# Kernel optimization log

Measured on AMD Instinct MI355X. Metric: run time of the kernel, lower is better.

## Reference

```python
import jax, jax.numpy as jnp
import numpy as np

C = 96        # d_model
DI = 192      # d_inner = 2*C
N = 16        # d_state
R = 6         # dt_rank = ceil(C/16)
K = 4         # scan directions
B_, H_, W_ = 2, 48, 48


def setup_inputs():
    key = jax.random.key(0)
    ks = jax.random.split(key, 12)
    def rn(k, shape, s=0.02):
        return jax.random.normal(k, shape, jnp.float32) * s
    # S4D-real A init and realistic dt bias (inverse softplus of dt in [1e-3, 1e-1])
    A = jnp.tile(jnp.arange(1, N + 1, dtype=jnp.float32), (K, DI, 1))
    dt = jax.random.uniform(ks[0], (K, DI), jnp.float32, 1e-3, 1e-1)
    inv_softplus_dt = dt + jnp.log(-jnp.expm1(-dt))
    return {
        "x": jax.random.normal(ks[1], (B_, C, H_, W_), jnp.float32),
        "ln1_w": jnp.ones((C,), jnp.float32), "ln1_b": jnp.zeros((C,), jnp.float32),
        "in_proj_w": rn(ks[2], (2 * DI, C)),
        "conv_w": rn(ks[3], (DI, 1, 3, 3), 0.1), "conv_b": jnp.zeros((DI,), jnp.float32),
        "x_proj_w": rn(ks[4], (K, R + 2 * N, DI)),
        "dt_proj_w": rn(ks[5], (K, DI, R), 0.1), "dt_proj_b": inv_softplus_dt,
        "A_log": jnp.log(A), "Ds": jnp.ones((K, DI), jnp.float32),
        "out_norm_w": jnp.ones((DI,), jnp.float32), "out_norm_b": jnp.zeros((DI,), jnp.float32),
        "out_proj_w": rn(ks[6], (C, DI)),
        "ln2_w": jnp.ones((C,), jnp.float32), "ln2_b": jnp.zeros((C,), jnp.float32),
        "fc1_w": rn(ks[7], (C, C)), "fc1_b": jnp.zeros((C,), jnp.float32),
        "fc2_w": rn(ks[8], (C, C)), "fc2_b": jnp.zeros((C,), jnp.float32),
        "proj_w": rn(ks[9], (1, C)), "proj_b": jnp.zeros((1,), jnp.float32),
    }


def _layernorm(x, w, b, eps=1e-5):
    mu = x.mean(-1, keepdims=True)
    var = x.var(-1, keepdims=True)
    return (x - mu) * jax.lax.rsqrt(var + eps) * w + b


def _selective_scan(u, delta, A, Bm, Cm, D):
    # u, delta: (B,K,D,L); A: (K,D,N); Bm, Cm: (B,K,N,L); D: (K,D)
    dA = jnp.exp(jnp.einsum('bkdl,kdn->lbkdn', delta, A))
    dBu = jnp.einsum('bkdl,bknl->lbkdn', delta * u, Bm)
    Ct = jnp.moveaxis(Cm, -1, 0)  # (L,B,K,N)
    h0 = jnp.zeros(dA.shape[1:], u.dtype)
    def step(h, inp):
        dA_t, dBu_t, C_t = inp
        h = dA_t * h + dBu_t
        y = jnp.einsum('bkdn,bkn->bkd', h, C_t)
        return h, y
    _, ys = jax.lax.scan(step, h0, (dA, dBu, Ct))
    y = jnp.moveaxis(ys, 0, -1)  # (B,K,D,L)
    return y + u * D[None, :, :, None]


def _ss2d(x, in_proj_w, conv_w, conv_b, x_proj_w, dt_proj_w, dt_proj_b,
          A_log, Ds, out_norm_w, out_norm_b, out_proj_w):
    Bsz, H, W, _ = x.shape
    L = H * W
    xz = x @ in_proj_w.T                      # (B,H,W,2*DI)
    xh, z = jnp.split(xz, 2, axis=-1)
    xc = xh.transpose(0, 3, 1, 2)             # (B,DI,H,W)
    xc = jax.lax.conv_general_dilated(
        xc, conv_w, (1, 1), ((1, 1), (1, 1)),
        feature_group_count=DI,
        dimension_numbers=('NCHW', 'OIHW', 'NCHW')) + conv_b[None, :, None, None]
    xc = jax.nn.silu(xc)
    # cross-scan: 4 directions (row-major, col-major, and their reverses)
    xf = xc.reshape(Bsz, DI, L)
    xt = xc.transpose(0, 1, 3, 2).reshape(Bsz, DI, L)
    xs2 = jnp.stack([xf, xt], axis=1)
    xs = jnp.concatenate([xs2, jnp.flip(xs2, axis=-1)], axis=1)   # (B,4,DI,L)
    x_dbl = jnp.einsum('bkdl,kcd->bkcl', xs, x_proj_w)
    dts, Bm, Cm = jnp.split(x_dbl, [R, R + N], axis=2)
    delta = jnp.einsum('bkrl,kdr->bkdl', dts, dt_proj_w) + dt_proj_b[None, :, :, None]
    delta = jax.nn.softplus(delta)
    A = -jnp.exp(A_log)
    out_y = _selective_scan(xs, delta, A, Bm, Cm, Ds)             # (B,4,DI,L)
    # cross-merge: undo flips/transposes and sum
    inv_y = jnp.flip(out_y[:, 2:4], axis=-1)
    wh_y = out_y[:, 1].reshape(Bsz, DI, W, H).transpose(0, 1, 3, 2).reshape(Bsz, DI, L)
    invwh_y = inv_y[:, 1].reshape(Bsz, DI, W, H).transpose(0, 1, 3, 2).reshape(Bsz, DI, L)
    y = out_y[:, 0] + inv_y[:, 0] + wh_y + invwh_y                # (B,DI,L)
    y = _layernorm(y.transpose(0, 2, 1), out_norm_w, out_norm_b).reshape(Bsz, H, W, DI)
    y = y * jax.nn.silu(z)
    return y @ out_proj_w.T


def reference(x, ln1_w, ln1_b, in_proj_w, conv_w, conv_b, x_proj_w, dt_proj_w,
              dt_proj_b, A_log, Ds, out_norm_w, out_norm_b, out_proj_w,
              ln2_w, ln2_b, fc1_w, fc1_b, fc2_w, fc2_b, proj_w, proj_b):
    xh = x.transpose(0, 2, 3, 1)   # (B,H,W,C)
    # VSSBlock (pre-norm): x = x + SS2D(LN(x)); x = x + MLP(LN(x))
    h1 = _layernorm(xh, ln1_w, ln1_b)
    xh = xh + _ss2d(h1, in_proj_w, conv_w, conv_b, x_proj_w, dt_proj_w,
                    dt_proj_b, A_log, Ds, out_norm_w, out_norm_b, out_proj_w)
    h2 = _layernorm(xh, ln2_w, ln2_b)
    xh = xh + (jax.nn.gelu(h2 @ fc1_w.T + fc1_b, approximate=False) @ fc2_w.T + fc2_b)
    # 1x1 conv projector + sigmoid
    y = xh @ proj_w.T + proj_b     # (B,H,W,1)
    return jax.nn.sigmoid(y).transpose(0, 3, 1, 2)
```

## Files before the change

kernel.cpp:

```cpp
#include <hip/hip_runtime.h>
#include <cstdint>

static constexpr int LSZ = 2304;
static constexpr int CBS = 96;
static constexpr int DIN = 192;
static constexpr int NST = 16;
static constexpr int HHT = 48;
static constexpr int WWD = 48;
static constexpr int CHN = 16;
static constexpr int CHL = 144;

static constexpr size_t OFF_XCONV = 0;
static constexpr size_t OFF_SILUZ = 884736;
static constexpr size_t OFF_XC    = 1769472;
static constexpr size_t OFF_XCT   = 2654208;
static constexpr size_t OFF_DTR   = 3538944;
static constexpr size_t OFF_BCT   = 3686400;
static constexpr size_t OFF_DELTA = 4276224;
static constexpr size_t OFF_YK    = 7815168;
static constexpr size_t OFF_XH1   = 11354112;
static constexpr size_t OFF_WT    = 11796480;

__device__ __forceinline__ float f4get(const float4& v, int i) {
    return i == 0 ? v.x : i == 1 ? v.y : i == 2 ? v.z : v.w;
}

__device__ __forceinline__ float rotadd16(float v) {
    int m;
    m = __builtin_amdgcn_update_dpp(0, __float_as_int(v), 0x128, 0xf, 0xf, false); v += __int_as_float(m);
    m = __builtin_amdgcn_update_dpp(0, __float_as_int(v), 0x124, 0xf, 0xf, false); v += __int_as_float(m);
    m = __builtin_amdgcn_update_dpp(0, __float_as_int(v), 0x122, 0xf, 0xf, false); v += __int_as_float(m);
    m = __builtin_amdgcn_update_dpp(0, __float_as_int(v), 0x121, 0xf, 0xf, false); v += __int_as_float(m);
    return v;
}

__global__ __launch_bounds__(256) void kPrep(const float* __restrict__ Wp,
    const float* __restrict__ Wo, const float* __restrict__ W1,
    const float* __restrict__ W2, float* __restrict__ wt) {
    int e = blockIdx.x * 256 + threadIdx.x;
    if (e < 36864) {
        int c = e / 384, t = e % 384;
        wt[e] = Wp[t * 96 + c];
    } else if (e < 55296) {
        int e2 = e - 36864; int dd = e2 / 96, cc = e2 % 96;
        wt[e] = Wo[cc * 192 + dd];
    } else if (e < 64512) {
        int e2 = e - 55296; int jj = e2 / 96, ii = e2 % 96;
        wt[e] = W1[ii * 96 + jj];
    } else if (e < 73728) {
        int e2 = e - 64512; int jj = e2 / 96, ii = e2 % 96;
        wt[e] = W2[ii * 96 + jj];
    }
}

__global__ __launch_bounds__(384) void kA(const float* __restrict__ x,
    const float* __restrict__ ln1w, const float* __restrict__ ln1b,
    const float* __restrict__ Wt, float* __restrict__ xconv, float* __restrict__ siluz) {
    int blk = blockIdx.x; int b = blk / 144; int s0 = (blk % 144) * 16;
    int tid = threadIdx.x;
    __shared__ float xln[96][20];
    __shared__ float mu16[16], ir16[16];
#pragma unroll
    for (int it = 0; it < 4; ++it) {
        int e = it * 384 + tid; int c = e >> 4, si = e & 15;
        xln[c][si] = x[((size_t)b * CBS + c) * LSZ + s0 + si];
    }
    __syncthreads();
    if (tid < 16) {
        float s1 = 0.f, s2 = 0.f;
#pragma unroll 8
        for (int c = 0; c < 96; ++c) { float v = xln[c][tid]; s1 += v; s2 += v * v; }
        float mu = s1 * (1.f / 96.f);
        mu16[tid] = mu; ir16[tid] = rsqrtf(s2 * (1.f / 96.f) - mu * mu + 1e-5f);
    }
    __syncthreads();
#pragma unroll
    for (int it = 0; it < 4; ++it) {
        int e = it * 384 + tid; int c = e >> 4, si = e & 15;
        xln[c][si] = (xln[c][si] - mu16[si]) * ir16[si] * ln1w[c] + ln1b[c];
    }
    __syncthreads();
    float acc[16];
#pragma unroll
    for (int i = 0; i < 16; ++i) acc[i] = 0.f;
    for (int c = 0; c < 96; ++c) {
        float wv = Wt[c * 384 + tid];
#pragma unroll
        for (int i = 0; i < 16; ++i) acc[i] = fmaf(wv, xln[c][i], acc[i]);
    }
    if (tid < DIN) {
        size_t base = ((size_t)b * DIN + tid) * LSZ + s0;
#pragma unroll
        for (int q = 0; q < 4; ++q) {
            float4 v = make_float4(acc[4 * q], acc[4 * q + 1], acc[4 * q + 2], acc[4 * q + 3]);
            *(float4*)(xconv + base + 4 * q) = v;
        }
    } else {
        int t = tid - DIN;
#pragma unroll
        for (int si = 0; si < 16; ++si) {
            float z = acc[si];
            siluz[((size_t)b * LSZ + s0 + si) * DIN + t] = z / (1.f + __expf(-z));
        }
    }
}

__global__ __launch_bounds__(256) void kB(const float* __restrict__ xconv,
    const float* __restrict__ cw, const float* __restrict__ cb,
    float* __restrict__ xc, float* __restrict__ xcT) {
    int bd = blockIdx.x;
    int d = bd % DIN;
    int tid = threadIdx.x;
    __shared__ float inp[2304];
    __shared__ float outp[48 * 49];
    const float* src = xconv + (size_t)bd * LSZ;
#pragma unroll
    for (int i = 0; i < 9; ++i) inp[i * 256 + tid] = src[i * 256 + tid];
    float w0 = cw[d * 9 + 0], w1 = cw[d * 9 + 1], w2 = cw[d * 9 + 2];
    float w3 = cw[d * 9 + 3], w4 = cw[d * 9 + 4], w5 = cw[d * 9 + 5];
    float w6 = cw[d * 9 + 6], w7 = cw[d * 9 + 7], w8 = cw[d * 9 + 8];
    float bias = cb[d];
    __syncthreads();
#pragma unroll
    for (int i = 0; i < 9; ++i) {
        int s = i * 256 + tid; int h = s / 48, w = s % 48;
        float acc = bias;
        bool hn = h > 0, hp = h < 47, wn = w > 0, wp = w < 47;
        if (hn) {
            if (wn) acc = fmaf(inp[s - 49], w0, acc);
            acc = fmaf(inp[s - 48], w1, acc);
            if (wp) acc = fmaf(inp[s - 47], w2, acc);
        }
        if (wn) acc = fmaf(inp[s - 1], w3, acc);
        acc = fmaf(inp[s], w4, acc);
        if (wp) acc = fmaf(inp[s + 1], w5, acc);
        if (hp) {
            if (wn) acc = fmaf(inp[s + 47], w6, acc);
            acc = fmaf(inp[s + 48], w7, acc);
            if (wp) acc = fmaf(inp[s + 49], w8, acc);
        }
        float r = acc / (1.f + __expf(-acc));
        xc[(size_t)bd * LSZ + s] = r;
        outp[h * 49 + w] = r;
    }
    __syncthreads();
#pragma unroll
    for (int i = 0; i < 9; ++i) {
        int p = i * 256 + tid;
        int w = p / 48, h = p % 48;
        xcT[(size_t)bd * LSZ + p] = outp[h * 49 + w];
    }
}

__global__ __launch_bounds__(256) void kC1(const float* __restrict__ xc,
    const float* __restrict__ xcT, const float* __restrict__ xpw,
    float* __restrict__ dtr, float* __restrict__ BCt) {
    int blk = blockIdx.x; int lt = blk % 36; int k = (blk / 36) & 3; int b = blk / 144;
    int l0 = lt * 64;
    int bk = b * 4 + k;
    __shared__ float xs[DIN][64];
    __shared__ float stage[64][33];
    const float* src = ((k & 1) ? xcT : xc) + (size_t)b * DIN * LSZ;
    bool fwd = (k < 2);
    int tid = threadIdx.x;
#pragma unroll
    for (int i = 0; i < 48; ++i) {
        int e = i * 256 + tid; int d = e >> 6, ll = e & 63;
        int l = l0 + ll; int sl = fwd ? l : (LSZ - 1 - l);
        xs[d][ll] = src[(size_t)d * LSZ + sl];
    }
    __syncthreads();
    int c0 = tid >> 6, ll = tid & 63;
    float acc[10];
#pragma unroll
    for (int j = 0; j < 10; ++j) acc[j] = 0.f;
    for (int d0 = 0; d0 < DIN; d0 += 16) {
        float xv[16];
#pragma unroll
        for (int i = 0; i < 16; ++i) xv[i] = xs[d0 + i][ll];
#pragma unroll
        for (int j = 0; j < 10; ++j) {
            int c = j * 4 + c0;
            if (c < 38) {
                const float4* wr = (const float4*)(xpw + ((size_t)(k * 38 + c)) * DIN + d0);
                float4 q0 = wr[0], q1 = wr[1], q2 = wr[2], q3 = wr[3];
                acc[j] += xv[0] * q0.x + xv[1] * q0.y + xv[2] * q0.z + xv[3] * q0.w
                        + xv[4] * q1.x + xv[5] * q1.y + xv[6] * q1.z + xv[7] * q1.w
                        + xv[8] * q2.x + xv[9] * q2.y + xv[10] * q2.z + xv[11] * q2.w
                        + xv[12] * q3.x + xv[13] * q3.y + xv[14] * q3.z + xv[15] * q3.w;
            }
        }
    }
#pragma unroll
    for (int j = 0; j < 10; ++j) {
        int c = j * 4 + c0;
        if (c < 6) {
            dtr[(size_t)bk * 8 * LSZ + (size_t)c * LSZ + l0 + ll] = acc[j];
        } else if (c < 38) {
            int n2 = (c < 22) ? (c - 6) : (16 + c - 22);
            stage[ll][n2] = acc[j];
        }
    }
    __syncthreads();
    float* dst = BCt + ((size_t)bk * LSZ + l0) * 32;
#pragma unroll
    for (int it = 0; it < 8; ++it) {
        int e = it * 256 + tid; int l = e >> 5, n2 = e & 31;
        dst[e] = stage[l][n2];
    }
}

__global__ __launch_bounds__(256) void kC2(const float* __restrict__ dtr,
    const float* __restrict__ dtw, const float* __restrict__ dtb, float* __restrict__ delta) {
    int blk = blockIdx.x; int lt = blk % 36; int k = (blk / 36) & 3; int b = blk / 144;
    int l0 = lt * 64;
    int bk = b * 4 + k;
    int tid = threadIdx.x;
    __shared__ float wsh[DIN * 6];
    __shared__ float bsh[DIN];
    for (int e = tid; e < 1152; e += 256) wsh[e] = dtw[k * 1152 + e];
    if (tid < DIN) bsh[tid] = dtb[k * DIN + tid];
    int dsub = tid >> 6, ll = tid & 63;
    float dr[6];
#pragma unroll
    for (int r = 0; r < 6; ++r) dr[r] = dtr[(size_t)bk * 8 * LSZ + (size_t)r * LSZ + l0 + ll];
    __syncthreads();
    for (int j = 0; j < 48; ++j) {
        int d = j * 4 + dsub;
        float acc = bsh[d];
#pragma unroll
        for (int r = 0; r < 6; ++r) acc = fmaf(dr[r], wsh[d * 6 + r], acc);
        float sp = (acc > 20.f) ? acc : log1pf(__expf(acc));
        delta[((size_t)(bk) * DIN + d) * LSZ + l0 + ll] = sp;
    }
}

__global__ __launch_bounds__(256, 4) void kD(const float* __restrict__ delta,
    const float* __restrict__ xc, const float* __restrict__ xcT,
    const float* __restrict__ BCt, const float* __restrict__ A_log, float* __restrict__ yk) {
    int g = blockIdx.x;
    int tid = threadIdx.x;
    int n = tid & 15; int c = tid >> 4;
    int d = g % DIN; int bk = g / DIN; int k = bk & 3; int b = bk >> 2;
    __shared__ float hfinL[256];
    __shared__ float sumdL[16];
    __shared__ float hinL[256];

    float An2 = -__expf(A_log[((size_t)(k * DIN + d)) * NST + n]) * 1.44269504f;
    const float* ub = ((k & 1) ? xcT : xc) + ((size_t)(b * DIN + d)) * LSZ;
    bool fwd = (k < 2);
    int l0 = c * CHL;
    const float* dp = delta + (size_t)g * LSZ + l0;
    const float* up = fwd ? (ub + l0) : (ub + (LSZ - 4) - l0);
    const float* bc = BCt + ((size_t)bk * LSZ + l0) * 32 + n;

    float h = 0.f, sd = 0.f;
    for (int j0 = 0; j0 < CHL; j0 += 4) {
        float4 dv = *(const float4*)(dp + j0);
        float4 uv;
        if (fwd) uv = *(const float4*)(up + j0);
        else { float4 tv = *(const float4*)(up - j0); uv = make_float4(tv.w, tv.z, tv.y, tv.x); }
#pragma unroll
        for (int jj = 0; jj < 4; ++jj) {
            float bn = bc[(j0 + jj) * 32];
            float dl = f4get(dv, jj);
            float da = __builtin_amdgcn_exp2f(dl * An2);
            h = fmaf(da, h, dl * f4get(uv, jj) * bn);
            sd += dl;
        }
    }
    hfinL[tid] = h;
    if (n == 0) sumdL[c] = sd;
    __syncthreads();

    if (tid < 16) {
        float hh = 0.f;
#pragma unroll
        for (int cc = 0; cc < 16; ++cc) {
            hinL[cc * 16 + tid] = hh;
            hh = fmaf(__builtin_amdgcn_exp2f(An2 * sumdL[cc]), hh, hfinL[cc * 16 + tid]);
        }
    }
    __syncthreads();

    h = hinL[tid];
    float* yo = yk + (size_t)g * LSZ + l0 + n;
    for (int m = 0; m < 9; ++m) {
        float ykeep = 0.f;
        for (int q = 0; q < 4; ++q) {
            int j0 = m * 16 + q * 4;
            float4 dv = *(const float4*)(dp + j0);
            float4 uv;
            if (fwd) uv = *(const float4*)(up + j0);
            else { float4 tv = *(const float4*)(up - j0); uv = make_float4(tv.w, tv.z, tv.y, tv.x); }
#pragma unroll
            for (int jj = 0; jj < 4; ++jj) {
                float bn = bc[(j0 + jj) * 32];
                float cn = bc[(j0 + jj) * 32 + 16];
                float dl = f4get(dv, jj);
                float da = __builtin_amdgcn_exp2f(dl * An2);
                h = fmaf(da, h, dl * f4get(uv, jj) * bn);
                float p = rotadd16(h * cn);
                ykeep = (n == q * 4 + jj) ? p : ykeep;
            }
        }
        yo[m * 16] = ykeep;
    }
}

__global__ __launch_bounds__(256) void kM(const float* __restrict__ yk,
    const float* __restrict__ xc, const float* __restrict__ Dsp, float* __restrict__ ym) {
    int blk = blockIdx.x;
    int b = blk / DIN; int d = blk % DIN;
    int tid = threadIdx.x;
    __shared__ float buf[4][2304];
    float Dsum = Dsp[d] + Dsp[DIN + d] + Dsp[2 * DIN + d] + Dsp[3 * DIN + d];
#pragma unroll
    for (int k = 0; k < 4; ++k) {
        const float* src = yk + ((size_t)((b * 4 + k) * DIN + d)) * LSZ;
#pragma unroll
        for (int i = 0; i < 9; ++i) buf[k][i * 256 + tid] = src[i * 256 + tid];
    }
    __syncthreads();
    const float* xrow = xc + ((size_t)(b * DIN + d)) * LSZ;
    float* dst = ym + ((size_t)blk) * LSZ;
#pragma unroll
    for (int i = 0; i < 9; ++i) {
        int s = i * 256 + tid; int hh = s / 48, ww = s % 48;
        int p = ww * 48 + hh;
        dst[s] = buf[0][s] + buf[2][2303 - s] + buf[1][p] + buf[3][2303 - p]
               + Dsum * xrow[s];
    }
}

__global__ __launch_bounds__(192) void kE(const float* __restrict__ ym,
    const float* __restrict__ siluz, const float* __restrict__ x,
    const float* __restrict__ onw, const float* __restrict__ onb,
    const float* __restrict__ WoT, float* __restrict__ xh1) {
    int blk = blockIdx.x; int b = blk / 144; int s0 = (blk % 144) * 16;
    int tid = threadIdx.x;
    __shared__ float yl[DIN][17];
    __shared__ float mu16[16], ir16[16];
#pragma unroll
    for (int it = 0; it < 16; ++it) {
        int e = it * 192 + tid; int d = e >> 4, si = e & 15;
        yl[d][si] = ym[((size_t)(b * DIN + d)) * LSZ + s0 + si];
    }
    __syncthreads();
    if (tid < 16) {
        float s1 = 0.f, s2 = 0.f;
        for (int c = 0; c < DIN; ++c) { float v = yl[c][tid]; s1 += v; s2 += v * v; }
        float mu = s1 * (1.f / 192.f);
        mu16[tid] = mu; ir16[tid] = rsqrtf(s2 * (1.f / 192.f) - mu * mu + 1e-5f);
    }
    __syncthreads();
#pragma unroll
    for (int si = 0; si < 16; ++si) {
        float v = yl[tid][si];
        v = (v - mu16[si]) * ir16[si] * onw[tid] + onb[tid];
        yl[tid][si] = v * siluz[((size_t)b * LSZ + s0 + si) * DIN + tid];
    }
    __syncthreads();
    int tp = tid % 96, half = tid / 96;
    float acc[8];
#pragma unroll
    for (int i = 0; i < 8; ++i) acc[i] = 0.f;
    for (int d2 = 0; d2 < DIN; ++d2) {
        float wv = WoT[d2 * 96 + tp];
#pragma unroll
        for (int i = 0; i < 8; ++i) acc[i] = fmaf(wv, yl[d2][half * 8 + i], acc[i]);
    }
#pragma unroll
    for (int i = 0; i < 8; ++i) {
        int si = half * 8 + i;
        xh1[((size_t)b * LSZ + s0 + si) * CBS + tp] =
            x[((size_t)b * CBS + tp) * LSZ + s0 + si] + acc[i];
    }
}

__global__ __launch_bounds__(192) void kF(const float* __restrict__ xh1,
    const float* __restrict__ l2w, const float* __restrict__ l2b,
    const float* __restrict__ W1T, const float* __restrict__ b1,
    const float* __restrict__ W2T, const float* __restrict__ b2,
    const float* __restrict__ pw, const float* __restrict__ pb, float* __restrict__ out) {
    int blk = blockIdx.x; int b = blk / 144; int s0 = (blk % 144) * 16;
    int tid = threadIdx.x;
    __shared__ float xo[96][17];
    __shared__ float aa[96][17];
    __shared__ float mu16[16], ir16[16];
#pragma unroll
    for (int it = 0; it < 8; ++it) {
        int e = it * 192 + tid; int si = e / 96, cc = e % 96;
        xo[cc][si] = xh1[((size_t)b * LSZ + s0 + si) * CBS + cc];
    }
    __syncthreads();
    if (tid < 16) {
        float s1 = 0.f, s2 = 0.f;
        for (int c = 0; c < 96; ++c) { float v = xo[c][tid]; s1 += v; s2 += v * v; }
        float mu = s1 * (1.f / 96.f);
        mu16[tid] = mu; ir16[tid] = rsqrtf(s2 * (1.f / 96.f) - mu * mu + 1e-5f);
    }
    __syncthreads();
#pragma unroll
    for (int it = 0; it < 8; ++it) {
        int e = it * 192 + tid; int si = e / 96, cc = e % 96;
        aa[cc][si] = (xo[cc][si] - mu16[si]) * ir16[si] * l2w[cc] + l2b[cc];
    }
    __syncthreads();
    int tp = tid % 96, half = tid / 96;
    float acc[8];
#pragma unroll
    for (int i = 0; i < 8; ++i) acc[i] = 0.f;
    for (int j = 0; j < 96; ++j) {
        float wv = W1T[j * 96 + tp];
#pragma unroll
        for (int i = 0; i < 8; ++i) acc[i] = fmaf(wv, aa[j][half * 8 + i], acc[i]);
    }
    __syncthreads();
#pragma unroll
    for (int i = 0; i < 8; ++i) {
        float tv = acc[i] + b1[tp];
        aa[tp][half * 8 + i] = 0.5f * tv * (1.f + erff(tv * 0.70710678118654752f));
    }
    __syncthreads();
    float acc2[8];
#pragma unroll
    for (int i = 0; i < 8; ++i) acc2[i] = 0.f;
    for (int j = 0; j < 96; ++j) {
        float wv = W2T[j * 96 + tp];
#pragma unroll
        for (int i = 0; i < 8; ++i) acc2[i] = fmaf(wv, aa[j][half * 8 + i], acc2[i]);
    }
    __syncthreads();
#pragma unroll
    for (int i = 0; i < 8; ++i) {
        float xf = xo[tp][half * 8 + i] + acc2[i] + b2[tp];
        aa[tp][half * 8 + i] = xf * pw[tp];
    }
    __syncthreads();
    if (tid < 16) {
        float ssum = 0.f;
        for (int c = 0; c < 96; ++c) ssum += aa[c][tid];
        out[(size_t)b * LSZ + s0 + tid] = 1.f / (1.f + __expf(-(ssum + pb[0])));
    }
}

extern "C" void kernel_launch(void* const* d_in, const int* in_sizes, int n_in,
                              void* d_out, int out_size, void* d_ws, size_t ws_size,
                              hipStream_t stream) {
    const float* x    = (const float*)d_in[0];
    const float* ln1w = (const float*)d_in[1];
    const float* ln1b = (const float*)d_in[2];
    const float* Wp   = (const float*)d_in[3];
    const float* cw   = (const float*)d_in[4];
    const float* cb   = (const float*)d_in[5];
    const float* xpw  = (const float*)d_in[6];
    const float* dtw  = (const float*)d_in[7];
    const float* dtb  = (const float*)d_in[8];
    const float* Alog = (const float*)d_in[9];
    const float* Dsp  = (const float*)d_in[10];
    const float* onw  = (const float*)d_in[11];
    const float* onb  = (const float*)d_in[12];
    const float* Wo   = (const float*)d_in[13];
    const float* l2w  = (const float*)d_in[14];
    const float* l2b  = (const float*)d_in[15];
    const float* W1   = (const float*)d_in[16];
    const float* b1   = (const float*)d_in[17];
    const float* W2   = (const float*)d_in[18];
    const float* b2   = (const float*)d_in[19];
    const float* pw   = (const float*)d_in[20];
    const float* pb   = (const float*)d_in[21];

    float* ws    = (float*)d_ws;
    float* xconv = ws + OFF_XCONV;
    float* ym    = ws + OFF_XCONV;
    float* siluz = ws + OFF_SILUZ;
    float* xc    = ws + OFF_XC;
    float* xcT   = ws + OFF_XCT;
    float* dtr   = ws + OFF_DTR;
    float* BCt   = ws + OFF_BCT;
    float* delta = ws + OFF_DELTA;
    float* yk    = ws + OFF_YK;
    float* xh1   = ws + OFF_XH1;
    float* wt    = ws + OFF_WT;
    float* WoT   = wt + 36864;
    float* W1T   = wt + 55296;
    float* W2T   = wt + 64512;

    kPrep<<<288, 256, 0, stream>>>(Wp, Wo, W1, W2, wt);
    kA<<<288, 384, 0, stream>>>(x, ln1w, ln1b, wt, xconv, siluz);
    kB<<<384, 256, 0, stream>>>(xconv, cw, cb, xc, xcT);
    kC1<<<288, 256, 0, stream>>>(xc, xcT, xpw, dtr, BCt);
    kC2<<<288, 256, 0, stream>>>(dtr, dtw, dtb, delta);
    kD<<<1536, 256, 0, stream>>>(delta, xc, xcT, BCt, Alog, yk);
    kM<<<384, 256, 0, stream>>>(yk, xc, Dsp, ym);
    kE<<<288, 192, 0, stream>>>(ym, siluz, x, onw, onb, WoT, xh1);
    kF<<<288, 192, 0, stream>>>(xh1, l2w, l2b, W1T, b1, W2T, b2, pw, pb, (float*)d_out);
}
```

Before: 185.0 us.

## Fuse dt projection into x_proj kernel, fuse out_proj with MLP, rechunk scan

Merges kC1 and kC2 so the dt_rank projection stays in shared memory and softplus delta is computed in the same block, removing the dtr round trip and one launch. Merges kE and kF so the residual xh1 never goes to global memory. The scan kernel moves from 16 chunks of 144 to 24 chunks of 96 with 384-thread blocks for more parallelism per (b,k,d). kM pads its shared buffer to stride 49 to avoid bank conflicts on transposed reads. Costs are more shared memory per block in the fused kernels and a longer serial cross-chunk combine.

```diff
diff --git a/kernel.cpp b/kernel.cpp
--- a/kernel.cpp
+++ b/kernel.cpp
@@ -7,18 +7,16 @@
 static constexpr int NST = 16;
 static constexpr int HHT = 48;
 static constexpr int WWD = 48;
-static constexpr int CHN = 16;
-static constexpr int CHL = 144;
+static constexpr int CHN = 24;
+static constexpr int CHL = 96;
 
 static constexpr size_t OFF_XCONV = 0;
 static constexpr size_t OFF_SILUZ = 884736;
 static constexpr size_t OFF_XC    = 1769472;
 static constexpr size_t OFF_XCT   = 2654208;
-static constexpr size_t OFF_DTR   = 3538944;
 static constexpr size_t OFF_BCT   = 3686400;
 static constexpr size_t OFF_DELTA = 4276224;
 static constexpr size_t OFF_YK    = 7815168;
-static constexpr size_t OFF_XH1   = 11354112;
 static constexpr size_t OFF_WT    = 11796480;
 
 __device__ __forceinline__ float f4get(const float4& v, int i) {
@@ -152,17 +150,23 @@
     }
 }
 
-__global__ __launch_bounds__(256) void kC1(const float* __restrict__ xc,
+__global__ __launch_bounds__(256) void kC(const float* __restrict__ xc,
     const float* __restrict__ xcT, const float* __restrict__ xpw,
-    float* __restrict__ dtr, float* __restrict__ BCt) {
+    const float* __restrict__ dtw, const float* __restrict__ dtb,
+    float* __restrict__ BCt, float* __restrict__ delta) {
     int blk = blockIdx.x; int lt = blk % 36; int k = (blk / 36) & 3; int b = blk / 144;
     int l0 = lt * 64;
     int bk = b * 4 + k;
     __shared__ float xs[DIN][64];
     __shared__ float stage[64][33];
+    __shared__ float dtrL[6][64];
+    __shared__ float wsh[DIN * 6];
+    __shared__ float bshL[DIN];
     const float* src = ((k & 1) ? xcT : xc) + (size_t)b * DIN * LSZ;
     bool fwd = (k < 2);
     int tid = threadIdx.x;
+    for (int e = tid; e < 1152; e += 256) wsh[e] = dtw[k * 1152 + e];
+    if (tid < DIN) bshL[tid] = dtb[k * DIN + tid];
 #pragma unroll
     for (int i = 0; i < 48; ++i) {
         int e = i * 256 + tid; int d = e >> 6, ll = e & 63;
@@ -195,7 +199,7 @@
     for (int j = 0; j < 10; ++j) {
         int c = j * 4 + c0;
         if (c < 6) {
-            dtr[(size_t)bk * 8 * LSZ + (size_t)c * LSZ + l0 + ll] = acc[j];
+            dtrL[c][ll] = acc[j];
         } else if (c < 38) {
             int n2 = (c < 22) ? (c - 6) : (16 + c - 22);
             stage[ll][n2] = acc[j];
@@ -205,46 +209,34 @@
     float* dst = BCt + ((size_t)bk * LSZ + l0) * 32;
 #pragma unroll
     for (int it = 0; it < 8; ++it) {
-        int e = it * 256 + tid; int l = e >> 5, n2 = e & 31;
+        int e = it * 256 + tid;
+        int l = e >> 5, n2 = e & 31;
         dst[e] = stage[l][n2];
     }
-}
-
-__global__ __launch_bounds__(256) void kC2(const float* __restrict__ dtr,
-    const float* __restrict__ dtw, const float* __restrict__ dtb, float* __restrict__ delta) {
-    int blk = blockIdx.x; int lt = blk % 36; int k = (blk / 36) & 3; int b = blk / 144;
-    int l0 = lt * 64;
-    int bk = b * 4 + k;
-    int tid = threadIdx.x;
-    __shared__ float wsh[DIN * 6];
-    __shared__ float bsh[DIN];
-    for (int e = tid; e < 1152; e += 256) wsh[e] = dtw[k * 1152 + e];
-    if (tid < DIN) bsh[tid] = dtb[k * DIN + tid];
-    int dsub = tid >> 6, ll = tid & 63;
+    int dsub = tid >> 6;
     float dr[6];
 #pragma unroll
-    for (int r = 0; r < 6; ++r) dr[r] = dtr[(size_t)bk * 8 * LSZ + (size_t)r * LSZ + l0 + ll];
-    __syncthreads();
+    for (int r = 0; r < 6; ++r) dr[r] = dtrL[r][ll];
     for (int j = 0; j < 48; ++j) {
         int d = j * 4 + dsub;
-        float acc = bsh[d];
-#pragma unroll
-        for (int r = 0; r < 6; ++r) acc = fmaf(dr[r], wsh[d * 6 + r], acc);
-        float sp = (acc > 20.f) ? acc : log1pf(__expf(acc));
-        delta[((size_t)(bk) * DIN + d) * LSZ + l0 + ll] = sp;
-    }
-}
-
-__global__ __launch_bounds__(256, 4) void kD(const float* __restrict__ delta,
+        float a2 = bshL[d];
+#pragma unroll
+        for (int r = 0; r < 6; ++r) a2 = fmaf(dr[r], wsh[d * 6 + r], a2);
+        float sp = (a2 > 20.f) ? a2 : log1pf(__expf(a2));
+        delta[((size_t)bk * DIN + d) * LSZ + l0 + ll] = sp;
+    }
+}
+
+__global__ __launch_bounds__(384, 4) void kD(const float* __restrict__ delta,
     const float* __restrict__ xc, const float* __restrict__ xcT,
     const float* __restrict__ BCt, const float* __restrict__ A_log, float* __restrict__ yk) {
     int g = blockIdx.x;
     int tid = threadIdx.x;
     int n = tid & 15; int c = tid >> 4;
     int d = g % DIN; int bk = g / DIN; int k = bk & 3; int b = bk >> 2;
-    __shared__ float hfinL[256];
-    __shared__ float sumdL[16];
-    __shared__ float hinL[256];
+    __shared__ float hfinL[384];
+    __shared__ float sumdL[CHN];
+    __shared__ float hinL[384];
 
     float An2 = -__expf(A_log[((size_t)(k * DIN + d)) * NST + n]) * 1.44269504f;
     const float* ub = ((k & 1) ? xcT : xc) + ((size_t)(b * DIN + d)) * LSZ;
@@ -276,7 +268,7 @@
     if (tid < 16) {
         float hh = 0.f;
 #pragma unroll
-        for (int cc = 0; cc < 16; ++cc) {
+        for (int cc = 0; cc < CHN; ++cc) {
             hinL[cc * 16 + tid] = hh;
             hh = fmaf(__builtin_amdgcn_exp2f(An2 * sumdL[cc]), hh, hfinL[cc * 16 + tid]);
         }
@@ -285,7 +277,7 @@
 
     h = hinL[tid];
     float* yo = yk + (size_t)g * LSZ + l0 + n;
-    for (int m = 0; m < 9; ++m) {
+    for (int m = 0; m < CHL / 16; ++m) {
         float ykeep = 0.f;
         for (int q = 0; q < 4; ++q) {
             int j0 = m * 16 + q * 4;
@@ -313,13 +305,16 @@
     int blk = blockIdx.x;
     int b = blk / DIN; int d = blk % DIN;
     int tid = threadIdx.x;
-    __shared__ float buf[4][2304];
+    __shared__ float buf[4][48 * 49];
     float Dsum = Dsp[d] + Dsp[DIN + d] + Dsp[2 * DIN + d] + Dsp[3 * DIN + d];
 #pragma unroll
-    for (int k = 0; k < 4; ++k) {
-        const float* src = yk + ((size_t)((b * 4 + k) * DIN + d)) * LSZ;
-#pragma unroll
-        for (int i = 0; i < 9; ++i) buf[k][i * 256 + tid] = src[i * 256 + tid];
+    for (int kk = 0; kk < 4; ++kk) {
+        const float* src = yk + ((size_t)((b * 4 + kk) * DIN + d)) * LSZ;
+#pragma unroll
+        for (int i = 0; i < 9; ++i) {
+            int s = i * 256 + tid;
+            buf[kk][s + s / 48] = src[s];
+        }
     }
     __syncthreads();
     const float* xrow = xc + ((size_t)(b * DIN + d)) * LSZ;
@@ -327,19 +322,27 @@
 #pragma unroll
     for (int i = 0; i < 9; ++i) {
         int s = i * 256 + tid; int hh = s / 48, ww = s % 48;
-        int p = ww * 48 + hh;
-        dst[s] = buf[0][s] + buf[2][2303 - s] + buf[1][p] + buf[3][2303 - p]
-               + Dsum * xrow[s];
-    }
-}
-
-__global__ __launch_bounds__(192) void kE(const float* __restrict__ ym,
+        float v0 = buf[0][hh * 49 + ww];
+        float v2 = buf[2][(47 - hh) * 49 + (47 - ww)];
+        float v1 = buf[1][ww * 49 + hh];
+        float v3 = buf[3][(47 - ww) * 49 + (47 - hh)];
+        dst[s] = v0 + v2 + v1 + v3 + Dsum * xrow[s];
+    }
+}
+
+__global__ __launch_bounds__(192) void kEF(const float* __restrict__ ym,
     const float* __restrict__ siluz, const float* __restrict__ x,
     const float* __restrict__ onw, const float* __restrict__ onb,
-    const float* __restrict__ WoT, float* __restrict__ xh1) {
+    const float* __restrict__ WoT,
+    const float* __restrict__ l2w, const float* __restrict__ l2b,
+    const float* __restrict__ W1T, const float* __restrict__ b1,
+    const float* __restrict__ W2T, const float* __restrict__ b2,
+    const float* __restrict__ pw, const float* __restrict__ pb, float* __restrict__ out) {
     int blk = blockIdx.x; int b = blk / 144; int s0 = (blk % 144) * 16;
     int tid = threadIdx.x;
     __shared__ float yl[DIN][17];
+    __shared__ float xo[96][17];
+    __shared__ float aa[96][17];
     __shared__ float mu16[16], ir16[16];
 #pragma unroll
     for (int it = 0; it < 16; ++it) {
@@ -362,36 +365,20 @@
     }
     __syncthreads();
     int tp = tid % 96, half = tid / 96;
-    float acc[8];
-#pragma unroll
-    for (int i = 0; i < 8; ++i) acc[i] = 0.f;
-    for (int d2 = 0; d2 < DIN; ++d2) {
-        float wv = WoT[d2 * 96 + tp];
-#pragma unroll
-        for (int i = 0; i < 8; ++i) acc[i] = fmaf(wv, yl[d2][half * 8 + i], acc[i]);
-    }
-#pragma unroll
-    for (int i = 0; i < 8; ++i) {
-        int si = half * 8 + i;
-        xh1[((size_t)b * LSZ + s0 + si) * CBS + tp] =
-            x[((size_t)b * CBS + tp) * LSZ + s0 + si] + acc[i];
-    }
-}
-
-__global__ __launch_bounds__(192) void kF(const float* __restrict__ xh1,
-    const float* __restrict__ l2w, const float* __restrict__ l2b,
-    const float* __restrict__ W1T, const float* __restrict__ b1,
-    const float* __restrict__ W2T, const float* __restrict__ b2,
-    const float* __restrict__ pw, const float* __restrict__ pb, float* __restrict__ out) {
-    int blk = blockIdx.x; int b = blk / 144; int s0 = (blk % 144) * 16;
-    int tid = threadIdx.x;
-    __shared__ float xo[96][17];
-    __shared__ float aa[96][17];
-    __shared__ float mu16[16], ir16[16];
-#pragma unroll
-    for (int it = 0; it < 8; ++it) {
-        int e = it * 192 + tid; int si = e / 96, cc = e % 96;
-        xo[cc][si] = xh1[((size_t)b * LSZ + s0 + si) * CBS + cc];
+    {
+        float acc[8];
+#pragma unroll
+        for (int i = 0; i < 8; ++i) acc[i] = 0.f;
+        for (int d2 = 0; d2 < DIN; ++d2) {
+            float wv = WoT[d2 * 96 + tp];
+#pragma unroll
+            for (int i = 0; i < 8; ++i) acc[i] = fmaf(wv, yl[d2][half * 8 + i], acc[i]);
+        }
+#pragma unroll
+        for (int i = 0; i < 8; ++i) {
+            int si = half * 8 + i;
+            xo[tp][si] = x[((size_t)b * CBS + tp) * LSZ + s0 + si] + acc[i];
+        }
     }
     __syncthreads();
     if (tid < 16) {
@@ -407,7 +394,6 @@
         aa[cc][si] = (xo[cc][si] - mu16[si]) * ir16[si] * l2w[cc] + l2b[cc];
     }
     __syncthreads();
-    int tp = tid % 96, half = tid / 96;
     float acc[8];
 #pragma unroll
     for (int i = 0; i < 8; ++i) acc[i] = 0.f;
@@ -477,11 +463,9 @@
     float* siluz = ws + OFF_SILUZ;
     float* xc    = ws + OFF_XC;
     float* xcT   = ws + OFF_XCT;
-    float* dtr   = ws + OFF_DTR;
     float* BCt   = ws + OFF_BCT;
     float* delta = ws + OFF_DELTA;
     float* yk    = ws + OFF_YK;
-    float* xh1   = ws + OFF_XH1;
     float* wt    = ws + OFF_WT;
     float* WoT   = wt + 36864;
     float* W1T   = wt + 55296;
@@ -490,10 +474,9 @@
     kPrep<<<288, 256, 0, stream>>>(Wp, Wo, W1, W2, wt);
     kA<<<288, 384, 0, stream>>>(x, ln1w, ln1b, wt, xconv, siluz);
     kB<<<384, 256, 0, stream>>>(xconv, cw, cb, xc, xcT);
-    kC1<<<288, 256, 0, stream>>>(xc, xcT, xpw, dtr, BCt);
-    kC2<<<288, 256, 0, stream>>>(dtr, dtw, dtb, delta);
-    kD<<<1536, 256, 0, stream>>>(delta, xc, xcT, BCt, Alog, yk);
+    kC<<<288, 256, 0, stream>>>(xc, xcT, xpw, dtw, dtb, BCt, delta);
+    kD<<<1536, 384, 0, stream>>>(delta, xc, xcT, BCt, Alog, yk);
     kM<<<384, 256, 0, stream>>>(yk, xc, Dsp, ym);
-    kE<<<288, 192, 0, stream>>>(ym, siluz, x, onw, onb, WoT, xh1);
-    kF<<<288, 192, 0, stream>>>(xh1, l2w, l2b, W1T, b1, W2T, b2, pw, pb, (float*)d_out);
-}
+    kEF<<<288, 192, 0, stream>>>(ym, siluz, x, onw, onb, WoT,
+                                 l2w, l2b, W1T, b1, W2T, b2, pw, pb, (float*)d_out);
+}
```

Result: slower. 399.8 us (+116.1%).
